# Kernel tuning notes

Hardware: AMD Instinct MI355X
Metric: run time of the kernel (lower is better)

The kernel has to match this reference:

```python
import jax, jax.numpy as jnp
import numpy as np

B, S, E, H = 2, 2048, 1024, 16
D = E // H

def setup_inputs() -> dict:
    key = jax.random.key(0)
    k1, k2, k3, k4, k5 = jax.random.split(key, 5)
    s = 1.0 / np.sqrt(E)
    return {
        "x": jax.random.normal(k1, (B, S, E), dtype=jnp.float32),
        "wv_w": jax.random.uniform(k2, (E, E), jnp.float32, -s, s),
        "wv_b": jax.random.uniform(k3, (E,), jnp.float32, -s, s),
        "wo_w": jax.random.uniform(k4, (E, E), jnp.float32, -s, s),
        "wo_b": jax.random.uniform(k5, (E,), jnp.float32, -s, s),
    }

def reference(x, wv_w, wv_b, wo_w, wo_b):
    b, s_len, e = x.shape
    # v projection -> (B, H, S, D)
    v = (x @ wv_w.T + wv_b).reshape(b, s_len, H, D).transpose(0, 2, 1, 3)
    # causal mask: True above diagonal (blocked); m = inclusive lower triangle
    causal = jnp.triu(jnp.ones((s_len, s_len), dtype=bool), k=1)
    m = (~causal).astype(x.dtype)
    # per-batch min-max scaling over (h, s, d)
    v_min = v.min(axis=(1, 2, 3), keepdims=True)
    v_max = v.max(axis=(1, 2, 3), keepdims=True)
    v_scaled = (v - v_min) / (v_max - v_min + 1e-8)
    # genetic fitness: masked mean pooling + reciprocal-mean normalization
    summed = jnp.einsum('ij,bhjd->bhid', m, v_scaled)  # (B,H,S,D)
    counts = jnp.maximum(m.sum(axis=1), 1.0)[None, None, :, None]
    phi = summed / counts
    denom = phi + 0.5
    sum_inv = (1.0 / denom).sum(axis=-1, keepdims=True)
    gene_fitness = 1.0 / (denom * sum_inv)  # weight, (B,H,S,D)
    # organism fitness scores
    org = jnp.einsum('bhjd,bhid->bhij', v_scaled, gene_fitness)
    org = jnp.where(causal[None, None], -jnp.inf, org)
    attn = jax.nn.softmax(org, axis=-1)
    out = jnp.einsum('bhij,bhjd->bhid', attn, v)
    out = out.transpose(0, 2, 1, 3).reshape(b, s_len, e)
    return out @ wo_w.T + wo_b
```

## Files before the change

kernel.cpp:

```cpp
#include <hip/hip_runtime.h>
#include <hip/hip_bf16.h>

#define B_ 2
#define S_ 2048
#define E_ 1024
#define H_ 16
#define D_ 64
#define M_ 4096

typedef __bf16 bf16_t;
typedef bf16_t bf16x8 __attribute__((ext_vector_type(8)));
typedef float f32x4 __attribute__((ext_vector_type(4)));
typedef unsigned int u32;

__device__ __forceinline__ f32x4 mfma16(bf16x8 a, bf16x8 b, f32x4 c) {
    return __builtin_amdgcn_mfma_f32_16x16x32_bf16(a, b, c, 0, 0, 0);
}
__device__ __forceinline__ unsigned short f2bf(float f) {
    unsigned int u = __float_as_uint(f);
    unsigned int r = (u + 0x7fffu + ((u >> 16) & 1u)) >> 16;
    return (unsigned short)r;
}
__device__ __forceinline__ float bf2f(unsigned short s) {
    return __uint_as_float(((unsigned int)s) << 16);
}
__device__ __forceinline__ u32 cvt_pk_bf16(float lo, float hi) {
    u32 r;
    asm("v_cvt_pk_bf16_f32 %0, %1, %2" : "=v"(r) : "v"(lo), "v"(hi));
    return r;
}
__device__ __forceinline__ unsigned int fenc(float x) {
    unsigned int u = __float_as_uint(x);
    return (u & 0x80000000u) ? ~u : (u | 0x80000000u);
}
__device__ __forceinline__ float fdec(unsigned int u) {
    return __uint_as_float((u & 0x80000000u) ? (u ^ 0x80000000u) : ~u);
}
__device__ __forceinline__ void gload16(const void* g, void* l) {
    __builtin_amdgcn_global_load_lds((const __attribute__((address_space(1))) u32*)g,
                                     (__attribute__((address_space(3))) u32*)l, 16, 0, 0);
}

__global__ __launch_bounds__(256) void k_prep(const float* __restrict__ x,
                                              const float* __restrict__ wv,
                                              const float* __restrict__ wo,
                                              unsigned short* __restrict__ xd,
                                              unsigned short* __restrict__ wvd,
                                              unsigned short* __restrict__ wod,
                                              unsigned int* __restrict__ mm) {
    int bid = blockIdx.x, tid = threadIdx.x;
    if (bid == 0 && tid < 2) { mm[tid * 2] = 0xFFFFFFFFu; mm[tid * 2 + 1] = 0u; }
    const float* src;
    unsigned short* dst;
    int i, rows;
    if (bid < 2048) { src = x;  dst = xd;  i = bid * 256 + tid;          rows = 4096; }
    else if (bid < 2560) { src = wv; dst = wvd; i = (bid - 2048) * 256 + tid; rows = 1024; }
    else { src = wo; dst = wod; i = (bid - 2560) * 256 + tid; rows = 1024; }
    int m = (i * 8) >> 10, k = (i * 8) & 1023;
    int kt = k >> 6, ko = k & 63;
    const float4* s4 = (const float4*)src;
    float4 a = s4[2 * i], c = s4[2 * i + 1];
    uint4 o;
    o.x = cvt_pk_bf16(a.x, a.y);
    o.y = cvt_pk_bf16(a.z, a.w);
    o.z = cvt_pk_bf16(c.x, c.y);
    o.w = cvt_pk_bf16(c.z, c.w);
    *(uint4*)&dst[((size_t)kt * rows + m) * 64 + ko] = o;
}

template <int MODE>
__global__ __launch_bounds__(256, 1) void k_gemm(const unsigned short* __restrict__ A,
                                                 const unsigned short* __restrict__ Bm,
                                                 const float* __restrict__ bias,
                                                 unsigned short* __restrict__ outb,
                                                 unsigned short* __restrict__ vtb,
                                                 float* __restrict__ psum,
                                                 float* __restrict__ outf,
                                                 unsigned int* __restrict__ mm) {
    __shared__ __align__(16) unsigned short Asm[2][16384];
    __shared__ __align__(16) unsigned short Bsm[2][16384];
    const size_t AKT = (size_t)M_ * 64;
    const size_t BKT = (size_t)1024 * 64;
    int tid = threadIdx.x, lane = tid & 63, wv = tid >> 6;
    int wm = wv >> 1, wn = wv & 1;
    int m0 = blockIdx.x * 128, n0 = blockIdx.y * 128;
    int lrow = lane & 15, lgrp = lane >> 4, sw = lane & 7;
    int r8 = lane >> 3, ch = lane & 7;
    const unsigned short* Ag = A + (size_t)(m0 + wv * 8 + r8) * 64 + ((ch ^ r8) << 3);
    const unsigned short* Bg = Bm + (size_t)(n0 + wv * 8 + r8) * 64 + ((ch ^ r8) << 3);

#define STAGE(buf, tt)                                                                        \
    {                                                                                         \
        _Pragma("unroll") for (int k2 = 0; k2 < 2; ++k2)                                      \
            _Pragma("unroll") for (int i = 0; i < 4; ++i)                                     \
                gload16(Ag + (size_t)(2 * (tt) + k2) * AKT + (size_t)(i * 32) * 64,           \
                        &Asm[buf][k2 * 8192 + (i * 32 + wv * 8) * 64]);                       \
        _Pragma("unroll") for (int k2 = 0; k2 < 2; ++k2)                                      \
            _Pragma("unroll") for (int i = 0; i < 4; ++i)                                     \
                gload16(Bg + (size_t)(2 * (tt) + k2) * BKT + (size_t)(i * 32) * 64,           \
                        &Bsm[buf][k2 * 8192 + (i * 32 + wv * 8) * 64]);                       \
    }
#define COMPUTE(buf)                                                                          \
    {                                                                                         \
        _Pragma("unroll") for (int kh = 0; kh < 4; ++kh) {                                    \
            int kb = (kh >> 1) * 8192;                                                        \
            int cp = ((((kh & 1) << 2) | lgrp) ^ sw) << 3;                                    \
            bf16x8 af[4], bfr[4];                                                             \
            _Pragma("unroll") for (int mt = 0; mt < 4; ++mt)                                  \
                af[mt] = *(const bf16x8*)&Asm[buf][kb + (wm * 64 + mt * 16 + lrow) * 64 + cp];\
            _Pragma("unroll") for (int nt = 0; nt < 4; ++nt)                                  \
                bfr[nt] = *(const bf16x8*)&Bsm[buf][kb + (wn * 64 + nt * 16 + lrow) * 64 + cp];\
            _Pragma("unroll") for (int mt = 0; mt < 4; ++mt)                                  \
                _Pragma("unroll") for (int nt = 0; nt < 4; ++nt)                              \
                    acc[mt][nt] = mfma16(af[mt], bfr[nt], acc[mt][nt]);                       \
        }                                                                                     \
    }

    f32x4 acc[4][4];
#pragma unroll
    for (int i = 0; i < 4; ++i)
#pragma unroll
        for (int j = 0; j < 4; ++j) acc[i][j] = (f32x4){0.f, 0.f, 0.f, 0.f};

    STAGE(0, 0);
    STAGE(1, 1);
    for (int t = 0; t < 8; ++t) {
        if (t < 7) {
            asm volatile("s_waitcnt vmcnt(16)" ::: "memory");
        } else {
            asm volatile("s_waitcnt vmcnt(0)" ::: "memory");
        }
        __builtin_amdgcn_s_barrier();
        __builtin_amdgcn_sched_barrier(0);
        __builtin_amdgcn_s_setprio(1);
        COMPUTE(t & 1);
        __builtin_amdgcn_s_setprio(0);
        asm volatile("s_waitcnt lgkmcnt(0)" ::: "memory");
        __builtin_amdgcn_s_barrier();
        __builtin_amdgcn_sched_barrier(0);
        if (t < 6) STAGE(t & 1, t + 2);
    }
#undef STAGE
#undef COMPUTE

    float vmin = 1e30f, vmax = -1e30f;
#pragma unroll
    for (int nt = 0; nt < 4; ++nt) {
        int ncol = n0 + wn * 64 + nt * 16 + lrow;
        float bs = bias[ncol];
        float cs0 = 0.f, cs1 = 0.f;
#pragma unroll
        for (int mt = 0; mt < 4; ++mt) {
            unsigned int lo = 0, hi = 0;
#pragma unroll
            for (int r = 0; r < 4; ++r) {
                int mrow = m0 + wm * 64 + mt * 16 + lgrp * 4 + r;
                float val = acc[mt][nt][r] + bs;
                if constexpr (MODE == 0) {
                    vmin = fminf(vmin, val);
                    vmax = fmaxf(vmax, val);
                    if (mt < 2) cs0 += val; else cs1 += val;
                    int b = mrow >> 11, s = mrow & 2047, h = ncol >> 6, d = ncol & 63;
                    unsigned short bfv = f2bf(val);
                    outb[(size_t)((b * 16 + h) * 2048 + s) * 64 + d] = bfv;
                    if (r < 2) lo |= ((unsigned int)bfv) << (16 * r);
                    else       hi |= ((unsigned int)bfv) << (16 * (r - 2));
                } else {
                    outf[(size_t)mrow * 1024 + ncol] = val;
                }
            }
            if constexpr (MODE == 0) {
                int mrow0 = m0 + wm * 64 + mt * 16 + lgrp * 4;
                int b = mrow0 >> 11, s0 = mrow0 & 2047;
                int h = ncol >> 6, d = ncol & 63;
                uint2 pk; pk.x = lo; pk.y = hi;
                *(uint2*)&vtb[((size_t)(b * 16 + h) * 64 + d) * 2048 + s0] = pk;
            }
        }
        if constexpr (MODE == 0) {
            cs0 += __shfl_xor(cs0, 16);
            cs0 += __shfl_xor(cs0, 32);
            cs1 += __shfl_xor(cs1, 16);
            cs1 += __shfl_xor(cs1, 32);
            if (lgrp == 0) {
                int b = m0 >> 11, h = ncol >> 6, d = ncol & 63;
                int bh = b * 16 + h;
                int c0 = ((m0 & 2047) >> 5) + wm * 2;
                psum[((size_t)bh * 64 + c0) * 64 + d] = cs0;
                psum[((size_t)bh * 64 + c0 + 1) * 64 + d] = cs1;
            }
        }
    }
    if constexpr (MODE == 0) {
#pragma unroll
        for (int m = 1; m < 64; m <<= 1) {
            vmin = fminf(vmin, __shfl_xor(vmin, m));
            vmax = fmaxf(vmax, __shfl_xor(vmax, m));
        }
        if (lane == 0) {
            int b = m0 >> 11;
            atomicMin(&mm[b * 2], fenc(vmin));
            atomicMax(&mm[b * 2 + 1], fenc(vmax));
        }
    }
}

__global__ __launch_bounds__(64) void k_scan2(const float* __restrict__ ps,
                                              float* __restrict__ base) {
    int bh = blockIdx.x;
    int d = threadIdx.x;
    const float* p = ps + (size_t)bh * 64 * 64 + d;
    float* bo = base + (size_t)bh * 64 * 64 + d;
    float vals[64];
#pragma unroll
    for (int c = 0; c < 64; ++c) vals[c] = p[(size_t)c * 64];
    float run = 0.f;
#pragma unroll
    for (int c = 0; c < 64; ++c) {
        float t = vals[c];
        vals[c] = run;
        run += t;
    }
#pragma unroll
    for (int c = 0; c < 64; ++c) bo[(size_t)c * 64] = vals[c];
}

__global__ __launch_bounds__(256, 4) void k_attn(const unsigned short* __restrict__ vb,
                                                 const unsigned short* __restrict__ vt,
                                                 unsigned short* __restrict__ attn_out,
                                                 const float* __restrict__ base,
                                                 const unsigned int* __restrict__ mm) {
    __shared__ __align__(16) unsigned short Vsm[2][4096];
    __shared__ __align__(16) unsigned short Tsm[2][4096];
    __shared__ __align__(16) unsigned short plds[4][1024];
    int tid = threadIdx.x, lane = tid & 63, w = tid >> 6;
    int bid = blockIdx.x;
    int qt = 31 - (bid >> 5);
    int bh = ((bid & 7) << 2) | ((bid >> 3) & 3);
    int i0 = qt * 64 + w * 16;
    int lrow = lane & 15, lgrp = lane >> 4;
    int sx = lrow & 7;
    int r8 = lane >> 3, ch = lane & 7;

    int b = bh >> 4;
    float vmin = fdec(mm[b * 2]), vmax = fdec(mm[b * 2 + 1]);
    float ir = __fdividef(1.0f, vmax - vmin + 1e-8f);
    float C2 = (vmin * ir + 1.0f) * 1.4426950408889634f;

    const unsigned short* vbase = vb + (size_t)bh * S_ * 64;
    const unsigned short* tbase = vt + (size_t)bh * 64 * S_;

    {
        int c = i0 >> 5;
        float acc = base[((size_t)bh * 64 + c) * 64 + lane];
        const unsigned short* vrow = vbase + (size_t)(c << 5) * 64 + lane;
        if (w & 1) {
            float p0 = 0.f, p1 = 0.f, p2 = 0.f, p3 = 0.f;
#pragma unroll
            for (int r = 0; r < 16; r += 4) {
                p0 += bf2f(vrow[(size_t)r * 64]);
                p1 += bf2f(vrow[(size_t)(r + 1) * 64]);
                p2 += bf2f(vrow[(size_t)(r + 2) * 64]);
                p3 += bf2f(vrow[(size_t)(r + 3) * 64]);
            }
            acc += (p0 + p1) + (p2 + p3);
            vrow += 16 * 64;
        }
        float irl = ir * 1.4426950408889634f;
#pragma unroll 4
        for (int r = 0; r < 16; ++r) {
            acc += bf2f(vrow[(size_t)r * 64]);
            float phi = __fdividef(acc, (float)(i0 + r + 1));
            float inv = __fdividef(1.0f, (phi - vmin) * ir + 0.5f);
            float rs = inv;
#pragma unroll
            for (int m2 = 1; m2 < 64; m2 <<= 1) rs += __shfl_xor(rs, m2);
            plds[w][r * 64 + lane] = f2bf(__fdividef(inv, rs) * irl);
        }
    }
    bf16x8 ga0 = *(const bf16x8*)&plds[w][lrow * 64 + lgrp * 8];
    bf16x8 ga1 = *(const bf16x8*)&plds[w][lrow * 64 + 32 + lgrp * 8];

    const unsigned short* Vg = vbase + (size_t)(w * 8 + r8) * 64 + ((ch ^ r8) << 3);
    const unsigned short* Tg = tbase + (size_t)(w * 8 + r8) * S_ + ((ch ^ r8) << 3);

#define ASTAGE(buf, jt_)                                                                  \
    {                                                                                     \
        int j0s = (jt_) << 6;                                                             \
        _Pragma("unroll") for (int i = 0; i < 2; ++i)                                     \
            gload16(Vg + (size_t)(j0s + i * 32) * 64, &Vsm[buf][(i * 32 + w * 8) * 64]);  \
        _Pragma("unroll") for (int i = 0; i < 2; ++i)                                     \
            gload16(Tg + (size_t)(i * 32) * S_ + j0s, &Tsm[buf][(i * 32 + w * 8) * 64]);  \
    }

    f32x4 acc[4];
#pragma unroll
    for (int dn = 0; dn < 4; ++dn) acc[dn] = (f32x4){0.f, 0.f, 0.f, 0.f};
    float lsum = 0.f;

    int njt = qt + 1;
    ASTAGE(0, 0);
    for (int jt = 0; jt < njt; ++jt) {
        int cur = jt & 1;
        asm volatile("s_waitcnt vmcnt(0)" ::: "memory");
        __builtin_amdgcn_s_barrier();
        __builtin_amdgcn_sched_barrier(0);
        if (jt + 1 < njt) ASTAGE(cur ^ 1, jt + 1);
        int j0 = jt << 6;
        __builtin_amdgcn_s_setprio(1);
        f32x4 Sv[4];
#pragma unroll
        for (int n = 0; n < 4; ++n) {
            const unsigned short* vr = &Vsm[cur][(n * 16 + lrow) * 64];
            bf16x8 a0 = *(const bf16x8*)(vr + ((lgrp ^ sx) << 3));
            bf16x8 a1 = *(const bf16x8*)(vr + (((lgrp + 4) ^ sx) << 3));
            f32x4 c = (f32x4){0.f, 0.f, 0.f, 0.f};
            c = mfma16(a0, ga0, c);
            c = mfma16(a1, ga1, c);
            Sv[n] = c;
        }
        bool tail = (jt == njt - 1);
#pragma unroll
        for (int n = 0; n < 4; ++n) {
            float q0 = exp2f(Sv[n][0] - C2);
            float q1 = exp2f(Sv[n][1] - C2);
            float q2 = exp2f(Sv[n][2] - C2);
            float q3 = exp2f(Sv[n][3] - C2);
            if (tail) {
                int ii = i0 + lrow;
                int jj = j0 + n * 16 + 4 * lgrp;
                q0 = (jj     <= ii) ? q0 : 0.f;
                q1 = (jj + 1 <= ii) ? q1 : 0.f;
                q2 = (jj + 2 <= ii) ? q2 : 0.f;
                q3 = (jj + 3 <= ii) ? q3 : 0.f;
            }
            lsum += (q0 + q1) + (q2 + q3);
            uint2 pk;
            pk.x = cvt_pk_bf16(q0, q1);
            pk.y = cvt_pk_bf16(q2, q3);
            int chunk = 2 * n + (lgrp >> 1);
            *(uint2*)&plds[w][lrow * 64 + ((chunk ^ sx) << 3) + ((lgrp & 1) << 2)] = pk;
        }
#pragma unroll
        for (int chk = 0; chk < 2; ++chk) {
            int pc = ((chk * 4 + lgrp) ^ sx) << 3;
            bf16x8 pa = *(const bf16x8*)&plds[w][lrow * 64 + pc];
#pragma unroll
            for (int dn = 0; dn < 4; ++dn) {
                bf16x8 tf = *(const bf16x8*)&Tsm[cur][(dn * 16 + lrow) * 64 + pc];
                acc[dn] = mfma16(tf, pa, acc[dn]);
            }
        }
        __builtin_amdgcn_s_setprio(0);
    }
#undef ASTAGE
    lsum += __shfl_xor(lsum, 16);
    lsum += __shfl_xor(lsum, 32);
    lsum = __fdividef(1.0f, lsum);
    int bb = bh >> 4, h = bh & 15;
    int ii = i0 + lrow;
#pragma unroll
    for (int dn = 0; dn < 4; ++dn) {
        uint2 pk;
        pk.x = cvt_pk_bf16(acc[dn][0] * lsum, acc[dn][1] * lsum);
        pk.y = cvt_pk_bf16(acc[dn][2] * lsum, acc[dn][3] * lsum);
        *(uint2*)&attn_out[((size_t)h * M_ + bb * S_ + ii) * 64 + dn * 16 + lgrp * 4] = pk;
    }
}

extern "C" void kernel_launch(void* const* d_in, const int* in_sizes, int n_in,
                              void* d_out, int out_size, void* d_ws, size_t ws_size,
                              hipStream_t stream) {
    const float* x = (const float*)d_in[0];
    const float* wv_w = (const float*)d_in[1];
    const float* wv_b = (const float*)d_in[2];
    const float* wo_w = (const float*)d_in[3];
    const float* wo_b = (const float*)d_in[4];
    float* out = (float*)d_out;

    char* w = (char*)d_ws;
    unsigned short* x_bf = (unsigned short*)(w);
    unsigned short* wv_bf = (unsigned short*)(w + 8388608);
    unsigned short* wo_bf = (unsigned short*)(w + 10485760);
    unsigned short* v_bf = (unsigned short*)(w + 12582912);
    unsigned short* vt_bf = (unsigned short*)(w + 20971520);
    float* ps = (float*)(w + 29360128);
    float* base = (float*)(w + 29884416);
    unsigned short* a_bf = (unsigned short*)(w + 54525952);
    unsigned int* mm = (unsigned int*)(w + 62914560);
    if (ws_size < 62914576) return;

    k_prep<<<3072, 256, 0, stream>>>(x, wv_w, wo_w, x_bf, wv_bf, wo_bf, mm);
    k_gemm<0><<<dim3(32, 8), 256, 0, stream>>>(x_bf, wv_bf, wv_b, v_bf, vt_bf, ps, nullptr, mm);
    k_scan2<<<32, 64, 0, stream>>>(ps, base);
    k_attn<<<1024, 256, 0, stream>>>(v_bf, vt_bf, a_bf, base, mm);
    k_gemm<1><<<dim3(32, 8), 256, 0, stream>>>(a_bf, wo_bf, wo_b, nullptr, nullptr, nullptr, out, nullptr);
}
```

Before: 117.0 us.

## Fold chunk-prefix scan into attention kernel and batch phi computation

Removes the separate k_scan2 launch that built exclusive prefix sums of per-chunk column sums. Each attention wave now sums the needed chunk partials directly from the psum buffer, up to 63 strided loads per lane. The per-row phi/inverse computation is also restructured: all 16 rows are loaded and processed first, then the shuffle reductions run, which exposes more independent work. This trades one launch and a global round trip for redundant summation work inside every attention block.

Result: no change. 117.2 us (+0.2%).

```diff
diff --git a/kernel.cpp b/kernel.cpp
--- a/kernel.cpp
+++ b/kernel.cpp
@@ -205,30 +205,10 @@
     }
 }
 
-__global__ __launch_bounds__(64) void k_scan2(const float* __restrict__ ps,
-                                              float* __restrict__ base) {
-    int bh = blockIdx.x;
-    int d = threadIdx.x;
-    const float* p = ps + (size_t)bh * 64 * 64 + d;
-    float* bo = base + (size_t)bh * 64 * 64 + d;
-    float vals[64];
-#pragma unroll
-    for (int c = 0; c < 64; ++c) vals[c] = p[(size_t)c * 64];
-    float run = 0.f;
-#pragma unroll
-    for (int c = 0; c < 64; ++c) {
-        float t = vals[c];
-        vals[c] = run;
-        run += t;
-    }
-#pragma unroll
-    for (int c = 0; c < 64; ++c) bo[(size_t)c * 64] = vals[c];
-}
-
 __global__ __launch_bounds__(256, 4) void k_attn(const unsigned short* __restrict__ vb,
                                                  const unsigned short* __restrict__ vt,
                                                  unsigned short* __restrict__ attn_out,
-                                                 const float* __restrict__ base,
+                                                 const float* __restrict__ psum,
                                                  const unsigned int* __restrict__ mm) {
     __shared__ __align__(16) unsigned short Vsm[2][4096];
     __shared__ __align__(16) unsigned short Tsm[2][4096];
@@ -252,9 +232,19 @@
 
     {
         int c = i0 >> 5;
-        float acc = base[((size_t)bh * 64 + c) * 64 + lane];
+        const float* pp = psum + (size_t)bh * 64 * 64 + lane;
+        float b0 = 0.f, b1 = 0.f, b2 = 0.f, b3 = 0.f;
+        int cc = 0;
+        for (; cc + 4 <= c; cc += 4) {
+            b0 += pp[(size_t)cc * 64];
+            b1 += pp[(size_t)(cc + 1) * 64];
+            b2 += pp[(size_t)(cc + 2) * 64];
+            b3 += pp[(size_t)(cc + 3) * 64];
+        }
+        for (; cc < c; ++cc) b0 += pp[(size_t)cc * 64];
+        float acc = (b0 + b1) + (b2 + b3);
         const unsigned short* vrow = vbase + (size_t)(c << 5) * 64 + lane;
-        if (w & 1) {
+        if (i0 & 16) {
             float p0 = 0.f, p1 = 0.f, p2 = 0.f, p3 = 0.f;
 #pragma unroll
             for (int r = 0; r < 16; r += 4) {
@@ -266,16 +256,23 @@
             acc += (p0 + p1) + (p2 + p3);
             vrow += 16 * 64;
         }
+        float vvv[16];
+#pragma unroll
+        for (int r = 0; r < 16; ++r) vvv[r] = bf2f(vrow[(size_t)r * 64]);
+        float invv[16];
+#pragma unroll
+        for (int r = 0; r < 16; ++r) {
+            acc += vvv[r];
+            float phi = __fdividef(acc, (float)(i0 + r + 1));
+            invv[r] = __fdividef(1.0f, (phi - vmin) * ir + 0.5f);
+        }
         float irl = ir * 1.4426950408889634f;
-#pragma unroll 4
+#pragma unroll
         for (int r = 0; r < 16; ++r) {
-            acc += bf2f(vrow[(size_t)r * 64]);
-            float phi = __fdividef(acc, (float)(i0 + r + 1));
-            float inv = __fdividef(1.0f, (phi - vmin) * ir + 0.5f);
-            float rs = inv;
+            float rs = invv[r];
 #pragma unroll
             for (int m2 = 1; m2 < 64; m2 <<= 1) rs += __shfl_xor(rs, m2);
-            plds[w][r * 64 + lane] = f2bf(__fdividef(inv, rs) * irl);
+            plds[w][r * 64 + lane] = f2bf(__fdividef(invv[r], rs) * irl);
         }
     }
     bf16x8 ga0 = *(const bf16x8*)&plds[w][lrow * 64 + lgrp * 8];
@@ -385,14 +382,12 @@
     unsigned short* v_bf = (unsigned short*)(w + 12582912);
     unsigned short* vt_bf = (unsigned short*)(w + 20971520);
     float* ps = (float*)(w + 29360128);
-    float* base = (float*)(w + 29884416);
     unsigned short* a_bf = (unsigned short*)(w + 54525952);
     unsigned int* mm = (unsigned int*)(w + 62914560);
     if (ws_size < 62914576) return;
 
     k_prep<<<3072, 256, 0, stream>>>(x, wv_w, wo_w, x_bf, wv_bf, wo_bf, mm);
     k_gemm<0><<<dim3(32, 8), 256, 0, stream>>>(x_bf, wv_bf, wv_b, v_bf, vt_bf, ps, nullptr, mm);
-    k_scan2<<<32, 64, 0, stream>>>(ps, base);
-    k_attn<<<1024, 256, 0, stream>>>(v_bf, vt_bf, a_bf, base, mm);
+    k_attn<<<1024, 256, 0, stream>>>(v_bf, vt_bf, a_bf, ps, mm);
     k_gemm<1><<<dim3(32, 8), 256, 0, stream>>>(a_bf, wo_bf, wo_b, nullptr, nullptr, nullptr, out, nullptr);
 }
```
